# Kernel tuning notes

Hardware: AMD Instinct MI355X
Metric: run time of the kernel (lower is better)

## Reference

```python
import jax, jax.numpy as jnp
import numpy as np

B, TQ, TK = 4, 128, 512
DQ = DK = DV = H = 1024


def setup_inputs() -> dict:
    key = jax.random.key(0)
    ks = jax.random.split(key, 7)
    s = 0.05  # keep tanh out of saturation
    return {
        "query": jax.random.normal(ks[0], (B, TQ, DQ), dtype=jnp.float32),
        "key": jax.random.normal(ks[1], (B, TK, DK), dtype=jnp.float32),
        "value": jax.random.normal(ks[2], (B, TK, DV), dtype=jnp.float32),
        "Wq": jax.random.normal(ks[3], (DQ, H), dtype=jnp.float32) * s,
        "bq": jax.random.normal(ks[4], (H,), dtype=jnp.float32) * s,
        "Wk": jax.random.normal(ks[5], (DK, H), dtype=jnp.float32) * s,
        "v": jax.random.normal(ks[6], (H,), dtype=jnp.float32) * s,
    }


def reference(query, key, value, Wq, bq, Wk, v):
    # additive (Bahdanau) attention
    wq = jnp.einsum("bqd,dh->bqh", query, Wq) + bq      # [B,Tq,H]
    uh = jnp.einsum("bkd,dh->bkh", key, Wk)             # [B,Tk,H]
    # broadcast add -> [B,Tq,Tk,H], tanh, project to scalar score
    scores = jnp.einsum("bqkh,h->bqk",
                        jnp.tanh(wq[:, :, None, :] + uh[:, None, :, :]), v)
    attn = jax.nn.softmax(scores, axis=-1)              # [B,Tq,Tk]
    h = jnp.einsum("bqk,bkv->bqv", attn, value)         # [B,Tq,Dv]
    return h, attn
```

## Files before the change

kernel.cpp:

```cpp
#include <hip/hip_runtime.h>
#include <hip/hip_bf16.h>

typedef float f32x4 __attribute__((ext_vector_type(4)));
typedef float f32x2 __attribute__((ext_vector_type(2)));
typedef short s16x8 __attribute__((ext_vector_type(8)));
typedef short s16x4 __attribute__((ext_vector_type(4)));

#define NB  4
#define NTQ 128
#define NTK 512
#define NH  1024

__device__ __forceinline__ unsigned short f2bf(float x) {
    unsigned u = __builtin_bit_cast(unsigned, x);
    u += 0x7FFFu + ((u >> 16) & 1u);
    return (unsigned short)(u >> 16);
}

#define K2E  2.8853900817779268f

#define GLD16(gp, lp) __builtin_amdgcn_global_load_lds( \
    (const __attribute__((address_space(1))) unsigned int*)(gp), \
    (__attribute__((address_space(3))) unsigned int*)(lp), 16, 0, 0)

__global__ __launch_bounds__(256) void prep_kernel(
    const float* __restrict__ Q, const float* __restrict__ K,
    const float* __restrict__ Wq, const float* __restrict__ Wk,
    const float* __restrict__ value,
    short* __restrict__ Qb, short* __restrict__ Kb,
    short* __restrict__ WqT, short* __restrict__ WkT, short* __restrict__ valT)
{
    const int t = threadIdx.x, bx = blockIdx.x;
    if (bx < 640) {
        const float* src; short* dst; size_t base;
        if (bx < 128) { src = Q; dst = Qb; base = (size_t)bx * 4096; }
        else          { src = K; dst = Kb; base = (size_t)(bx - 128) * 4096; }
        #pragma unroll
        for (int i = 0; i < 4; ++i) {
            const size_t off = base + (size_t)(i * 256 + t) * 4;
            const float4 vv = *(const float4*)(src + off);
            s16x4 o = { (short)f2bf(vv.x), (short)f2bf(vv.y),
                        (short)f2bf(vv.z), (short)f2bf(vv.w) };
            *(s16x4*)(dst + off) = o;
        }
        return;
    }
    __shared__ float tile[64][65];
    const int i = bx - 640;
    const float* src; short* dst; int Cs, Rs, r0, c0;
    if (i < 256)      { src = Wq; dst = WqT; Cs = 1024; Rs = 1024; r0 = (i >> 4) * 64; c0 = (i & 15) * 64; }
    else if (i < 512) { const int j = i - 256; src = Wk; dst = WkT; Cs = 1024; Rs = 1024; r0 = (j >> 4) * 64; c0 = (j & 15) * 64; }
    else {
        const int j = i - 512, b = j >> 7, ti = j & 127;
        src = value + (size_t)b * 512 * 1024; dst = valT + (size_t)b * 1024 * 512;
        Cs = 1024; Rs = 512; r0 = (ti >> 4) * 64; c0 = (ti & 15) * 64;
    }
    {
        const int c = (t & 15) * 4;
        #pragma unroll
        for (int it = 0; it < 4; ++it) {
            const int r = (t >> 4) + it * 16;
            const float4 vv = *(const float4*)(src + (size_t)(r0 + r) * Cs + c0 + c);
            tile[r][c + 0] = vv.x; tile[r][c + 1] = vv.y;
            tile[r][c + 2] = vv.z; tile[r][c + 3] = vv.w;
        }
    }
    __syncthreads();
    {
        const int r = (t & 15) * 4;
        #pragma unroll
        for (int it = 0; it < 4; ++it) {
            const int c = (t >> 4) + it * 16;
            s16x4 o = { (short)f2bf(tile[r + 0][c]), (short)f2bf(tile[r + 1][c]),
                        (short)f2bf(tile[r + 2][c]), (short)f2bf(tile[r + 3][c]) };
            *(s16x4*)(dst + (size_t)(c0 + c) * Rs + r0 + r) = o;
        }
    }
}

__global__ __launch_bounds__(256) void mm_kernel(
    const short* __restrict__ Qb, const short* __restrict__ Kb,
    const short* __restrict__ WqT, const short* __restrict__ WkT,
    const float* __restrict__ bq,
    float* __restrict__ Ea_out, unsigned short* __restrict__ EbT)
{
    __shared__ short ldsA[2][128][64];
    __shared__ short ldsB[2][64][64];
    const int t = threadIdx.x;
    const int bx0 = blockIdx.x;
    const int bx = (bx0 & 7) * 40 + (bx0 >> 3);
    const bool g1 = bx < 64;
    const short *A, *B; int m0, n0;
    if (g1) { A = Qb; B = WqT; m0 = (bx >> 4) * 128; n0 = (bx & 15) * 64; }
    else    { const int i = bx - 64; A = Kb; B = WkT; m0 = (i >> 4) * 128; n0 = (i & 15) * 64; }
    A += (size_t)m0 * 1024; B += (size_t)n0 * 1024;

    f32x4 acc[4][2];
    #pragma unroll
    for (int i = 0; i < 4; ++i)
        #pragma unroll
        for (int j = 0; j < 2; ++j) acc[i][j] = f32x4{0.f, 0.f, 0.f, 0.f};

    const int lane = t & 63, wid = t >> 6;
    const int wr = wid >> 1, wc = wid & 1;
    const int fr = lane & 15, fko = (lane >> 4) * 16;

    #define STAGE_MM(buf, k0) do {                                              \
        _Pragma("unroll")                                                       \
        for (int it = 0; it < 4; ++it) {                                        \
            const int idx = it * 256 + t;                                       \
            const int row = idx >> 3, c16 = idx & 7;                            \
            const int sc = c16 ^ (row & 7);                                     \
            GLD16(A + (size_t)row * 1024 + (k0) + sc * 8,                       \
                  &ldsA[buf][0][0] + idx * 8);                                  \
        }                                                                       \
        _Pragma("unroll")                                                       \
        for (int it = 0; it < 2; ++it) {                                        \
            const int idx = it * 256 + t;                                       \
            const int row = idx >> 3, c16 = idx & 7;                            \
            const int sc = c16 ^ (row & 7);                                     \
            GLD16(B + (size_t)row * 1024 + (k0) + sc * 8,                       \
                  &ldsB[buf][0][0] + idx * 8);                                  \
        }                                                                       \
    } while (0)

    #define COMPUTE_MM(buf) do {                                                \
        _Pragma("unroll")                                                       \
        for (int kk = 0; kk < 2; ++kk) {                                        \
            s16x8 af[4], bfv[2];                                                \
            _Pragma("unroll")                                                   \
            for (int i = 0; i < 4; ++i) {                                       \
                const int rowA = wr * 64 + i * 16 + fr;                         \
                int offA = rowA * 128 + kk * 64 + fko; offA ^= (rowA & 7) << 4; \
                af[i] = *(const s16x8*)((const char*)&ldsA[buf][0][0] + offA);  \
            }                                                                   \
            _Pragma("unroll")                                                   \
            for (int ni = 0; ni < 2; ++ni) {                                    \
                const int rowB = wc * 32 + ni * 16 + fr;                        \
                int offB = rowB * 128 + kk * 64 + fko; offB ^= (rowB & 7) << 4; \
                bfv[ni] = *(const s16x8*)((const char*)&ldsB[buf][0][0] + offB);\
            }                                                                   \
            _Pragma("unroll")                                                   \
            for (int mi = 0; mi < 4; ++mi)                                      \
                _Pragma("unroll")                                               \
                for (int ni = 0; ni < 2; ++ni)                                  \
                    acc[mi][ni] = __builtin_amdgcn_mfma_f32_16x16x32_bf16(      \
                                      af[mi], bfv[ni], acc[mi][ni], 0, 0, 0);   \
        }                                                                       \
    } while (0)

    STAGE_MM(0, 0);
    __syncthreads();
    int cur = 0;
    for (int s = 0; s < 15; ++s) {
        STAGE_MM(cur ^ 1, (s + 1) * 64);
        COMPUTE_MM(cur);
        __syncthreads();
        cur ^= 1;
    }
    COMPUTE_MM(cur);

    const int row0 = (lane >> 4) * 4;
    if (g1) {
        #pragma unroll
        for (int ni = 0; ni < 2; ++ni) {
            const int n = n0 + wc * 32 + ni * 16 + fr;
            const float bias = bq[n];
            #pragma unroll
            for (int mi = 0; mi < 4; ++mi) {
                const int m = m0 + wr * 64 + mi * 16 + row0;
                #pragma unroll
                for (int j = 0; j < 4; ++j)
                    Ea_out[(size_t)(m + j) * 1024 + n] =
                        __builtin_amdgcn_exp2f(K2E * (acc[mi][ni][j] + bias));
            }
        }
    } else {
        #pragma unroll
        for (int mi = 0; mi < 4; ++mi) {
            const int m = m0 + wr * 64 + mi * 16 + row0;
            const int b = m >> 9, kk = m & 511;
            #pragma unroll
            for (int ni = 0; ni < 2; ++ni) {
                const int n = n0 + wc * 32 + ni * 16 + fr;
                s16x4 ev;
                #pragma unroll
                for (int j = 0; j < 4; ++j)
                    ev[j] = (short)f2bf(__builtin_amdgcn_exp2f(K2E * acc[mi][ni][j]));
                *(s16x4*)&EbT[((size_t)b * 1024 + n) * 512 + kk] = ev;
            }
        }
    }
    #undef STAGE_MM
    #undef COMPUTE_MM
}

__global__ __launch_bounds__(1024) void scores_softmax(
    const unsigned short* __restrict__ EbT, const float* __restrict__ Ea,
    const float* __restrict__ v,
    float* __restrict__ attn_out, short* __restrict__ attnb)
{
    __shared__ float4 s_eav[1024];
    __shared__ float2 s_part2[512];
    __shared__ float2 s_red[8];
    const int t = threadIdx.x, bx = blockIdx.x;
    const int b = bx >> 6, q2 = bx & 63;
    const int bq0 = b * 128 + q2 * 2;
    const int k = t & 511, hh = t >> 9;
    const int lane = t & 63, wid = t >> 6;

    s_eav[t] = make_float4(Ea[(size_t)(bq0 + 0) * 1024 + t],
                           Ea[(size_t)(bq0 + 1) * 1024 + t],
                           v[t], 0.f);
    __syncthreads();

    const int h0 = hh * 512;
    const unsigned short* up = EbT + ((size_t)b * 1024 + h0) * 512 + k;
    f32x2 acc = {0.f, 0.f};
    #pragma unroll 8
    for (int h = 0; h < 512; ++h) {
        const unsigned ebb = up[(size_t)h * 512];
        const float eb = __builtin_bit_cast(float, ebb << 16);
        const float4 e = s_eav[h0 + h];
        f32x2 p = f32x2{e.x, e.y} * eb + 1.0f;
        f32x2 r = {__builtin_amdgcn_rcpf(p.x), __builtin_amdgcn_rcpf(p.y)};
        acc += r * e.z;
    }
    if (hh == 1) s_part2[k] = make_float2(acc.x, acc.y);
    __syncthreads();

    f32x2 z = {0.f, 0.f};
    if (hh == 0) {
        const float2 o = s_part2[k];
        z = (acc + f32x2{o.x, o.y}) * -2.0f;
    }

    f32x2 m = z;
    #pragma unroll
    for (int off = 32; off > 0; off >>= 1) {
        m.x = fmaxf(m.x, __shfl_xor(m.x, off, 64));
        m.y = fmaxf(m.y, __shfl_xor(m.y, off, 64));
    }
    if (hh == 0 && lane == 0) s_red[wid] = make_float2(m.x, m.y);
    __syncthreads();
    float mx0 = s_red[0].x, mx1 = s_red[0].y;
    #pragma unroll
    for (int w = 1; w < 8; ++w) {
        mx0 = fmaxf(mx0, s_red[w].x);
        mx1 = fmaxf(mx1, s_red[w].y);
    }
    const float p0 = __expf(z.x - mx0);
    const float p1 = __expf(z.y - mx1);
    __syncthreads();

    float s0l = p0, s1l = p1;
    #pragma unroll
    for (int off = 32; off > 0; off >>= 1) {
        s0l += __shfl_xor(s0l, off, 64);
        s1l += __shfl_xor(s1l, off, 64);
    }
    if (hh == 0 && lane == 0) s_red[wid] = make_float2(s0l, s1l);
    __syncthreads();
    if (hh == 0) {
        float s0 = 0.f, s1 = 0.f;
        #pragma unroll
        for (int w = 0; w < 8; ++w) { s0 += s_red[w].x; s1 += s_red[w].y; }
        const float a0 = p0 * (1.0f / s0);
        const float a1 = p1 * (1.0f / s1);
        attn_out[(size_t)(bq0 + 0) * 512 + k] = a0;
        attn_out[(size_t)(bq0 + 1) * 512 + k] = a1;
        attnb[(size_t)(bq0 + 0) * 512 + k] = (short)f2bf(a0);
        attnb[(size_t)(bq0 + 1) * 512 + k] = (short)f2bf(a1);
    }
}

__global__ __launch_bounds__(256) void pv_gemm(
    const short* __restrict__ attnb, const short* __restrict__ valT,
    float* __restrict__ outh)
{
    __shared__ short ldsA[2][128][64];
    __shared__ short ldsB[2][64][64];
    const int t = threadIdx.x, bx = blockIdx.x;
    const int b = bx >> 4, nt = bx & 15;
    const int n0 = nt * 64;
    const short* A = attnb + (size_t)b * 128 * 512;
    const short* B = valT + (size_t)b * 1024 * 512 + (size_t)n0 * 512;

    f32x4 acc[4][2];
    #pragma unroll
    for (int i = 0; i < 4; ++i)
        #pragma unroll
        for (int j = 0; j < 2; ++j) acc[i][j] = f32x4{0.f, 0.f, 0.f, 0.f};

    const int lane = t & 63, wid = t >> 6;
    const int wr = wid >> 1, wc = wid & 1;
    const int fr = lane & 15, fko = (lane >> 4) * 16;

    #define STAGE_PV(buf, k0) do {                                              \
        _Pragma("unroll")                                                       \
        for (int it = 0; it < 4; ++it) {                                        \
            const int idx = it * 256 + t;                                       \
            const int row = idx >> 3, c16 = idx & 7;                            \
            const int sc = c16 ^ (row & 7);                                     \
            GLD16(A + (size_t)row * 512 + (k0) + sc * 8,                        \
                  &ldsA[buf][0][0] + idx * 8);                                  \
        }                                                                       \
        _Pragma("unroll")                                                       \
        for (int it = 0; it < 2; ++it) {                                        \
            const int idx = it * 256 + t;                                       \
            const int row = idx >> 3, c16 = idx & 7;                            \
            const int sc = c16 ^ (row & 7);                                     \
            GLD16(B + (size_t)row * 512 + (k0) + sc * 8,                        \
                  &ldsB[buf][0][0] + idx * 8);                                  \
        }                                                                       \
    } while (0)

    #define COMPUTE_PV(buf) do {                                                \
        _Pragma("unroll")                                                       \
        for (int kk = 0; kk < 2; ++kk) {                                        \
            s16x8 af[4], bfv[2];                                                \
            _Pragma("unroll")                                                   \
            for (int i = 0; i < 4; ++i) {                                       \
                const int rowA = wr * 64 + i * 16 + fr;                         \
                int offA = rowA * 128 + kk * 64 + fko; offA ^= (rowA & 7) << 4; \
                af[i] = *(const s16x8*)((const char*)&ldsA[buf][0][0] + offA);  \
            }                                                                   \
            _Pragma("unroll")                                                   \
            for (int ni = 0; ni < 2; ++ni) {                                    \
                const int rowB = wc * 32 + ni * 16 + fr;                        \
                int offB = rowB * 128 + kk * 64 + fko; offB ^= (rowB & 7) << 4; \
                bfv[ni] = *(const s16x8*)((const char*)&ldsB[buf][0][0] + offB);\
            }                                                                   \
            _Pragma("unroll")                                                   \
            for (int mi = 0; mi < 4; ++mi)                                      \
                _Pragma("unroll")                                               \
                for (int ni = 0; ni < 2; ++ni)                                  \
                    acc[mi][ni] = __builtin_amdgcn_mfma_f32_16x16x32_bf16(      \
                                      af[mi], bfv[ni], acc[mi][ni], 0, 0, 0);   \
        }                                                                       \
    } while (0)

    STAGE_PV(0, 0);
    __syncthreads();
    int cur = 0;
    for (int s = 0; s < 7; ++s) {
        STAGE_PV(cur ^ 1, (s + 1) * 64);
        COMPUTE_PV(cur);
        __syncthreads();
        cur ^= 1;
    }
    COMPUTE_PV(cur);

    const int row0 = (lane >> 4) * 4;
    #pragma unroll
    for (int ni = 0; ni < 2; ++ni) {
        const int n = n0 + wc * 32 + ni * 16 + fr;
        #pragma unroll
        for (int mi = 0; mi < 4; ++mi) {
            const int m = wr * 64 + mi * 16 + row0;
            #pragma unroll
            for (int j = 0; j < 4; ++j)
                outh[(size_t)(b * 128 + m + j) * 1024 + n] = acc[mi][ni][j];
        }
    }
    #undef STAGE_PV
    #undef COMPUTE_PV
}

extern "C" void kernel_launch(void* const* d_in, const int* in_sizes, int n_in,
                              void* d_out, int out_size, void* d_ws, size_t ws_size,
                              hipStream_t stream)
{
    const float* query = (const float*)d_in[0];
    const float* key   = (const float*)d_in[1];
    const float* value = (const float*)d_in[2];
    const float* Wq    = (const float*)d_in[3];
    const float* bq    = (const float*)d_in[4];
    const float* Wk    = (const float*)d_in[5];
    const float* v     = (const float*)d_in[6];
    float* out = (float*)d_out;

    char* w = (char*)d_ws;
    float*          ws_Ea  = (float*)w;
    unsigned short* ws_EbT = (unsigned short*)(w + (2u << 20));
    short* Qb     = (short*)(w + (6u << 20));
    short* Kb     = (short*)(w + (7u << 20));
    short* WqT    = (short*)(w + (11u << 20));
    short* WkT    = (short*)(w + (13u << 20));
    short* valT   = (short*)(w + (15u << 20));
    short* attnb  = (short*)(w + (19u << 20));

    float* out_h    = out;
    float* out_attn = out + (size_t)NB * NTQ * NH;

    prep_kernel   <<<dim3(1664), dim3(256),  0, stream>>>(query, key, Wq, Wk, value,
                                                          Qb, Kb, WqT, WkT, valT);
    mm_kernel     <<<dim3(320),  dim3(256),  0, stream>>>(Qb, Kb, WqT, WkT, bq, ws_Ea, ws_EbT);
    scores_softmax<<<dim3(256),  dim3(1024), 0, stream>>>(ws_EbT, ws_Ea, v, out_attn, attnb);
    pv_gemm       <<<dim3(64),   dim3(256),  0, stream>>>(attnb, valT, out_h);
}
```

Before: 77.74 us.

## Load packed bf16 pairs and split H four ways in scores_softmax

The score kernel now has each thread read 32-bit words holding two adjacent k values of the exp(key) table, so global loads are wider and each LDS read of Ea/v is reused across four products. The hidden dimension is split across four thread groups instead of two, with partial sums reduced through shared memory. The softmax stage is reorganised so all 1024 threads work, each handling one (query, k) element, and the launch bound asks for a higher occupancy hint. The cost is a larger shared-memory partial buffer and a four-way reduction.

```diff
diff --git a/kernel.cpp b/kernel.cpp
--- a/kernel.cpp
+++ b/kernel.cpp
@@ -195,18 +195,19 @@
     #undef COMPUTE_MM
 }
 
-__global__ __launch_bounds__(1024) void scores_softmax(
+__global__ __launch_bounds__(1024, 8) void scores_softmax(
     const unsigned short* __restrict__ EbT, const float* __restrict__ Ea,
     const float* __restrict__ v,
     float* __restrict__ attn_out, short* __restrict__ attnb)
 {
     __shared__ float4 s_eav[1024];
-    __shared__ float2 s_part2[512];
-    __shared__ float2 s_red[8];
+    __shared__ float  s_part[4][2][512];
+    __shared__ float  s_red[16];
     const int t = threadIdx.x, bx = blockIdx.x;
     const int b = bx >> 6, q2 = bx & 63;
     const int bq0 = b * 128 + q2 * 2;
-    const int k = t & 511, hh = t >> 9;
+    const int kp = t & 255;
+    const int hq = t >> 8;
     const int lane = t & 63, wid = t >> 6;
 
     s_eav[t] = make_float4(Ea[(size_t)(bq0 + 0) * 1024 + t],
@@ -214,64 +215,56 @@
                            v[t], 0.f);
     __syncthreads();
 
-    const int h0 = hh * 512;
-    const unsigned short* up = EbT + ((size_t)b * 1024 + h0) * 512 + k;
-    f32x2 acc = {0.f, 0.f};
+    const int h0 = hq * 256;
+    const unsigned* up = (const unsigned*)(EbT + ((size_t)b * 1024 + h0) * 512) + kp;
+    f32x2 a0 = {0.f, 0.f};
+    f32x2 a1 = {0.f, 0.f};
     #pragma unroll 8
-    for (int h = 0; h < 512; ++h) {
-        const unsigned ebb = up[(size_t)h * 512];
-        const float eb = __builtin_bit_cast(float, ebb << 16);
+    for (int h = 0; h < 256; ++h) {
+        const unsigned ebb = up[(size_t)h * 256];
+        const float eb0 = __builtin_bit_cast(float, ebb << 16);
+        const float eb1 = __builtin_bit_cast(float, ebb & 0xFFFF0000u);
         const float4 e = s_eav[h0 + h];
-        f32x2 p = f32x2{e.x, e.y} * eb + 1.0f;
-        f32x2 r = {__builtin_amdgcn_rcpf(p.x), __builtin_amdgcn_rcpf(p.y)};
-        acc += r * e.z;
-    }
-    if (hh == 1) s_part2[k] = make_float2(acc.x, acc.y);
-    __syncthreads();
-
-    f32x2 z = {0.f, 0.f};
-    if (hh == 0) {
-        const float2 o = s_part2[k];
-        z = (acc + f32x2{o.x, o.y}) * -2.0f;
-    }
-
-    f32x2 m = z;
-    #pragma unroll
-    for (int off = 32; off > 0; off >>= 1) {
-        m.x = fmaxf(m.x, __shfl_xor(m.x, off, 64));
-        m.y = fmaxf(m.y, __shfl_xor(m.y, off, 64));
-    }
-    if (hh == 0 && lane == 0) s_red[wid] = make_float2(m.x, m.y);
-    __syncthreads();
-    float mx0 = s_red[0].x, mx1 = s_red[0].y;
-    #pragma unroll
-    for (int w = 1; w < 8; ++w) {
-        mx0 = fmaxf(mx0, s_red[w].x);
-        mx1 = fmaxf(mx1, s_red[w].y);
-    }
-    const float p0 = __expf(z.x - mx0);
-    const float p1 = __expf(z.y - mx1);
-    __syncthreads();
-
-    float s0l = p0, s1l = p1;
-    #pragma unroll
-    for (int off = 32; off > 0; off >>= 1) {
-        s0l += __shfl_xor(s0l, off, 64);
-        s1l += __shfl_xor(s1l, off, 64);
-    }
-    if (hh == 0 && lane == 0) s_red[wid] = make_float2(s0l, s1l);
-    __syncthreads();
-    if (hh == 0) {
-        float s0 = 0.f, s1 = 0.f;
-        #pragma unroll
-        for (int w = 0; w < 8; ++w) { s0 += s_red[w].x; s1 += s_red[w].y; }
-        const float a0 = p0 * (1.0f / s0);
-        const float a1 = p1 * (1.0f / s1);
-        attn_out[(size_t)(bq0 + 0) * 512 + k] = a0;
-        attn_out[(size_t)(bq0 + 1) * 512 + k] = a1;
-        attnb[(size_t)(bq0 + 0) * 512 + k] = (short)f2bf(a0);
-        attnb[(size_t)(bq0 + 1) * 512 + k] = (short)f2bf(a1);
-    }
+        f32x2 p0 = f32x2{eb0, eb1} * e.x + 1.0f;
+        f32x2 p1 = f32x2{eb0, eb1} * e.y + 1.0f;
+        f32x2 r0 = {__builtin_amdgcn_rcpf(p0.x), __builtin_amdgcn_rcpf(p0.y)};
+        f32x2 r1 = {__builtin_amdgcn_rcpf(p1.x), __builtin_amdgcn_rcpf(p1.y)};
+        a0 += r0 * e.z;
+        a1 += r1 * e.z;
+    }
+    *(f32x2*)&s_part[hq][0][kp * 2] = a0;
+    *(f32x2*)&s_part[hq][1][kp * 2] = a1;
+    __syncthreads();
+
+    const int kk = t & 511, qq = t >> 9;
+    const float z = -2.0f * (s_part[0][qq][kk] + s_part[1][qq][kk]
+                           + s_part[2][qq][kk] + s_part[3][qq][kk]);
+
+    float m = z;
+    #pragma unroll
+    for (int off = 32; off > 0; off >>= 1)
+        m = fmaxf(m, __shfl_xor(m, off, 64));
+    if (lane == 0) s_red[wid] = m;
+    __syncthreads();
+    float mx = s_red[qq * 8];
+    #pragma unroll
+    for (int w = 1; w < 8; ++w) mx = fmaxf(mx, s_red[qq * 8 + w]);
+    const float p = __expf(z - mx);
+    __syncthreads();
+
+    float sl = p;
+    #pragma unroll
+    for (int off = 32; off > 0; off >>= 1)
+        sl += __shfl_xor(sl, off, 64);
+    if (lane == 0) s_red[wid] = sl;
+    __syncthreads();
+    float s = 0.f;
+    #pragma unroll
+    for (int w = 0; w < 8; ++w) s += s_red[qq * 8 + w];
+
+    const float a = p * (1.0f / s);
+    attn_out[(size_t)(bq0 + qq) * 512 + kk] = a;
+    attnb[(size_t)(bq0 + qq) * 512 + kk] = (short)f2bf(a);
 }
 
 __global__ __launch_bounds__(256) void pv_gemm(
```

Measured after the change: 73.29 us. 5.7% less time.
